# Optimization experiments

Measured on AMD Instinct MI355X. Metric: run time of the kernel, lower is better.

Reference implementation:

```python
import jax, jax.numpy as jnp
import numpy as np

D = 1024   # input_dim
H = 4096   # hidden_dim
E = 8      # num_experts
K = 2      # top_k
LN_EPS = 1e-5


def setup_inputs() -> dict:
    key = jax.random.key(0)
    ks = jax.random.split(key, 6)
    x = jax.random.normal(ks[0], (2, 4096, D), dtype=jnp.float32)
    gate_w = jax.random.normal(ks[1], (D, E), dtype=jnp.float32) * 0.02
    ln_scale = jnp.ones((E, D), dtype=jnp.float32)
    ln_bias = jnp.zeros((E, D), dtype=jnp.float32)
    w1 = jax.random.normal(ks[2], (E, D, H), dtype=jnp.float32) * 0.02
    b1 = jnp.zeros((E, H), dtype=jnp.float32)
    w2 = jax.random.normal(ks[3], (E, H, D), dtype=jnp.float32) * 0.02
    b2 = jnp.zeros((E, D), dtype=jnp.float32)
    return {"x": x, "gate_w": gate_w, "ln_scale": ln_scale, "ln_bias": ln_bias,
            "w1": w1, "b1": b1, "w2": w2, "b2": b2}


def reference(x, gate_w, ln_scale, ln_bias, w1, b1, w2, b2):
    xs = x.reshape(-1, D)                       # [T, D]
    T = xs.shape[0]
    # gating: softmax logits -> top-k -> renormalize selected weights via softmax
    probs = jax.nn.softmax(xs @ gate_w, axis=-1)            # [T, E]
    wts, sel = jax.lax.top_k(probs, K)                      # [T, K]
    wts = jax.nn.softmax(wts, axis=-1).astype(x.dtype)      # [T, K]
    # dense combine weights per (token, expert): 0 if not selected
    comb = jnp.zeros((T, E), dtype=x.dtype).at[jnp.arange(T)[:, None], sel].add(wts)
    # LayerNorm stats are expert-independent; compute once
    mu = xs.mean(-1, keepdims=True)
    var = jnp.mean((xs - mu) ** 2, axis=-1, keepdims=True)
    xn = (xs - mu) * jax.lax.rsqrt(var + LN_EPS)            # [T, D]
    out = jnp.zeros_like(xs)
    for e in range(E):  # small fixed loop over experts
        h = xn * ln_scale[e] + ln_bias[e]                   # [T, D]
        h1 = jax.nn.gelu(h @ w1[e] + b1[e], approximate=False)  # [T, H]
        y = h1 @ w2[e] + b2[e]                              # [T, D]
        out = out + comb[:, e, None] * y
    return out.reshape(x.shape)
```

## Files before the change

### kernel.cpp

```cpp
#include <hip/hip_runtime.h>
#include <hip/hip_bf16.h>
#include <hip/hip_fp16.h>
#include <math.h>

#define T_TOK 8192
#define DIM   1024
#define HID   4096
#define NE    8
#define NT256 72
#define CAP_ROWS (NT256 * 256)

typedef _Float16 f16x8 __attribute__((ext_vector_type(8)));
typedef float    floatx4 __attribute__((ext_vector_type(4)));

__device__ __forceinline__ void gload_lds16(const void* g, void* l) {
    __builtin_amdgcn_global_load_lds(
        (const __attribute__((address_space(1))) void*)g,
        (__attribute__((address_space(3))) void*)l,
        16, 0, 0);
}

__device__ __forceinline__ float gelu_f(float v) {
    float u = v * (0.7978845608028654f + 0.03567740813636141f * v * v);
    float e = exp2f(2.8853900817779268f * u);
    float th = 1.f - 2.f / (e + 1.f);
    return 0.5f * v * (1.f + th);
}

__global__ __launch_bounds__(256) void gating_ln_kernel(
    const float* __restrict__ x, const float* __restrict__ gw,
    int* __restrict__ sel, float* __restrict__ wts,
    float* __restrict__ mu_arr, float* __restrict__ rstd_arr)
{
    int t = blockIdx.x;
    int tid = threadIdx.x;
    float4 xv = ((const float4*)(x + (size_t)t * DIM))[tid];
    float s  = xv.x + xv.y + xv.z + xv.w;
    float ss = xv.x*xv.x + xv.y*xv.y + xv.z*xv.z + xv.w*xv.w;
    float l[NE];
#pragma unroll
    for (int e = 0; e < NE; e++) l[e] = 0.f;
    int d0 = tid * 4;
    const float* xp = &xv.x;
#pragma unroll
    for (int j = 0; j < 4; j++) {
        float xj = xp[j];
        const float4* g = (const float4*)(gw + (size_t)(d0 + j) * NE);
        float4 g0 = g[0], g1 = g[1];
        l[0] += xj * g0.x; l[1] += xj * g0.y; l[2] += xj * g0.z; l[3] += xj * g0.w;
        l[4] += xj * g1.x; l[5] += xj * g1.y; l[6] += xj * g1.z; l[7] += xj * g1.w;
    }
#pragma unroll
    for (int off = 32; off > 0; off >>= 1) {
        s  += __shfl_down(s, off);
        ss += __shfl_down(ss, off);
#pragma unroll
        for (int e = 0; e < NE; e++) l[e] += __shfl_down(l[e], off);
    }
    __shared__ float red[4][10];
    int lane = tid & 63, wv = tid >> 6;
    if (lane == 0) {
        red[wv][0] = s; red[wv][1] = ss;
        for (int e = 0; e < NE; e++) red[wv][2 + e] = l[e];
    }
    __syncthreads();
    if (tid == 0) {
        float S = 0.f, SS = 0.f, L[NE];
        for (int e = 0; e < NE; e++) L[e] = 0.f;
        for (int w = 0; w < 4; w++) {
            S += red[w][0]; SS += red[w][1];
            for (int e = 0; e < NE; e++) L[e] += red[w][2 + e];
        }
        float mu  = S * (1.f / DIM);
        float var = SS * (1.f / DIM) - mu * mu;
        float rstd = rsqrtf(var + 1e-5f);
        float lmax = L[0];
        for (int e = 1; e < NE; e++) lmax = fmaxf(lmax, L[e]);
        float den = 0.f;
        for (int e = 0; e < NE; e++) den += expf(L[e] - lmax);
        int i0 = 0; float b0 = L[0];
        for (int e = 1; e < NE; e++) if (L[e] > b0) { b0 = L[e]; i0 = e; }
        int i1 = -1; float b1v = -3.4e38f;
        for (int e = 0; e < NE; e++) if (e != i0 && L[e] > b1v) { b1v = L[e]; i1 = e; }
        float p0 = expf(b0 - lmax) / den;
        float p1 = expf(b1v - lmax) / den;
        float t1 = expf(p1 - p0);
        float w0 = 1.f / (1.f + t1);
        float w1 = t1 / (1.f + t1);
        sel[2*t] = i0;  sel[2*t+1] = i1;
        wts[2*t] = w0;  wts[2*t+1] = w1;
        mu_arr[t] = mu; rstd_arr[t] = rstd;
    }
}

__global__ __launch_bounds__(256) void hist_kernel(
    const int* __restrict__ sel, int* __restrict__ blockhist,
    unsigned short* __restrict__ lrank)
{
    int b = blockIdx.x, tid = threadIdx.x;
    int t = b * 256 + tid;
    int e0 = sel[2*t], e1 = sel[2*t+1];
    int lane = tid & 63, w = tid >> 6;
    __shared__ int c0[4][NE], c1[4][NE];
    unsigned long long below = (1ull << lane) - 1ull;
    int r0 = 0, r1 = 0;
#pragma unroll
    for (int e = 0; e < NE; e++) {
        unsigned long long m0 = __ballot(e0 == e);
        unsigned long long m1 = __ballot(e1 == e);
        if (lane == 0) { c0[w][e] = __popcll(m0); c1[w][e] = __popcll(m1); }
        if (e0 == e) r0 = __popcll(m0 & below);
        if (e1 == e) r1 = __popcll(m1 & below);
    }
    __syncthreads();
    int base0 = 0, base1 = 0;
#pragma unroll
    for (int wp = 0; wp < 4; wp++) {
        if (wp < w) { base0 += c0[wp][e0]; base1 += c1[wp][e1]; }
        base1 += c0[wp][e1];
    }
    lrank[2*t]   = (unsigned short)(base0 + r0);
    lrank[2*t+1] = (unsigned short)(base1 + r1);
    if (tid < NE) {
        int sum = 0;
        for (int wp = 0; wp < 4; wp++) sum += c0[wp][tid] + c1[wp][tid];
        blockhist[b * NE + tid] = sum;
    }
}

__global__ __launch_bounds__(256) void scan_kernel(
    const int* __restrict__ blockhist, int* __restrict__ off, int* __restrict__ counts,
    int* __restrict__ babs, int* __restrict__ tile_expert)
{
    __shared__ int soff[NE + 1];
    __shared__ int stot[NE];
    int tid = threadIdx.x;
    if (tid < NE) {
        int tot = 0;
        for (int b = 0; b < 32; b++) tot += blockhist[b * NE + tid];
        stot[tid] = tot; counts[tid] = tot;
    }
    __syncthreads();
    if (tid == 0) {
        int o = 0;
        for (int e = 0; e < NE; e++) { soff[e] = o; off[e] = o; o += ((stot[e] + 255) >> 8) << 8; }
        soff[NE] = o; off[NE] = o;
    }
    __syncthreads();
    if (tid < NE) {
        int run = soff[tid];
        for (int b = 0; b < 32; b++) { babs[b * NE + tid] = run; run += blockhist[b * NE + tid]; }
    }
    int o = soff[NE];
    for (int i = tid; i < NT256; i += 256) {
        int pos = i * 256, e = -1;
        if (pos < o) {
            for (int j = 0; j < NE; j++)
                if (pos >= soff[j] && pos < soff[j + 1]) { e = j; break; }
        }
        tile_expert[i] = e;
    }
}

__global__ __launch_bounds__(256) void scatter_kernel(
    const float* __restrict__ x, const float* __restrict__ ln_s, const float* __restrict__ ln_b,
    const int* __restrict__ sel,
    const float* __restrict__ mu_arr, const float* __restrict__ rstd_arr,
    const int* __restrict__ babs, const unsigned short* __restrict__ lrank,
    _Float16* __restrict__ xg, int* __restrict__ slot_of)
{
    int t = blockIdx.x, tid = threadIdx.x;
    int b = t >> 8;
    int e0 = sel[2*t], e1 = sel[2*t+1];
    int s0 = babs[b * NE + e0] + (int)lrank[2*t];
    int s1 = babs[b * NE + e1] + (int)lrank[2*t+1];
    if (tid == 0) { slot_of[2*t] = s0; slot_of[2*t+1] = s1; }
    float4 xv = ((const float4*)(x + (size_t)t * DIM))[tid];
    float mu = mu_arr[t], rstd = rstd_arr[t];
    float xn0 = (xv.x - mu) * rstd, xn1 = (xv.y - mu) * rstd;
    float xn2 = (xv.z - mu) * rstd, xn3 = (xv.w - mu) * rstd;
#pragma unroll
    for (int k = 0; k < 2; k++) {
        int e = (k == 0) ? e0 : e1;
        int slot = (k == 0) ? s0 : s1;
        float4 sv = ((const float4*)(ln_s + (size_t)e * DIM))[tid];
        float4 bv = ((const float4*)(ln_b + (size_t)e * DIM))[tid];
        _Float16 hb[4];
        hb[0] = (_Float16)(xn0 * sv.x + bv.x);
        hb[1] = (_Float16)(xn1 * sv.y + bv.y);
        hb[2] = (_Float16)(xn2 * sv.z + bv.z);
        hb[3] = (_Float16)(xn3 * sv.w + bv.w);
        *(uint2*)(xg + (size_t)slot * DIM + tid * 4) = *(const uint2*)hb;
    }
}

__global__ __launch_bounds__(256) void transpose_cvt_kernel(
    const float* __restrict__ in, _Float16* __restrict__ out, int R, int C)
{
    __shared__ _Float16 tile[64][65];
    size_t ebase = (size_t)blockIdx.z * R * C;
    const float* inp = in + ebase + (size_t)(blockIdx.y * 64) * C + blockIdx.x * 64;
    _Float16* outp = out + ebase + (size_t)(blockIdx.x * 64) * R + blockIdx.y * 64;
    int t = threadIdx.x & 31, j0 = threadIdx.x >> 5;
    for (int j = j0; j < 64; j += 8) {
        float2 v = *(const float2*)(inp + (size_t)j * C + 2 * t);
        tile[j][2*t]   = (_Float16)v.x;
        tile[j][2*t+1] = (_Float16)v.y;
    }
    __syncthreads();
    for (int j = j0; j < 64; j += 8) {
        _Float16 pr[2] = { tile[2*t][j], tile[2*t+1][j] };
        *(unsigned int*)(outp + (size_t)j * R + 2 * t) = *(unsigned int*)pr;
    }
}


#define BAR() __builtin_amdgcn_s_barrier()
#define WAITLGKM() asm volatile("s_waitcnt lgkmcnt(0)" ::: "memory")
#define SCB() __builtin_amdgcn_sched_barrier(0)
#define VMC0() asm volatile("s_waitcnt vmcnt(0)" ::: "memory")
#define VMCN() do { if (LPB == 2) { asm volatile("s_waitcnt vmcnt(6)" ::: "memory"); } \
                    else          { asm volatile("s_waitcnt vmcnt(5)" ::: "memory"); } } while (0)

#define DSA(B_, MHI) do {                                                        \
    const char* p_ = smb + (B_) * (2 * BUFH) + (MHI) * 16384 + aob;              \
    _Pragma("unroll")                                                            \
    for (int mi_ = 0; mi_ < MH; ++mi_) {                                         \
        af[mi_][0] = *(const f16x8*)(p_ + mi_ * 2048 + kx0);                     \
        af[mi_][1] = *(const f16x8*)(p_ + mi_ * 2048 + kx1);                     \
    }                                                                            \
} while (0)

#define DSB(B_, NHI) do {                                                        \
    const char* p_ = smb + (B_) * (2 * BUFH) + (NHI) * (BN * 64) + bob;          \
    _Pragma("unroll")                                                            \
    for (int tn_ = 0; tn_ < 2; ++tn_) {                                          \
        bf[tn_][0] = *(const f16x8*)(p_ + tn_ * 2048 + kx0);                     \
        bf[tn_][1] = *(const f16x8*)(p_ + tn_ * 2048 + kx1);                     \
    }                                                                            \
} while (0)

#define STA(B_, KOFF, H_) do {                                                   \
    _Float16* d_ = smem + (B_) * BUFH + (H_) * 8192 + tid * 8;                   \
    gload_lds16(gA0 + (size_t)((H_) * (WM / 2)) * K + (KOFF), d_);               \
    gload_lds16(gA1 + (size_t)((H_) * (WM / 2)) * K + (KOFF), d_ + 4096);        \
} while (0)

#define STB(B_, KOFF, H_) do {                                                   \
    _Float16* d_ = smem + (B_) * BUFH + 16384 + (H_) * BHH + tid * 8;            \
    gload_lds16(gB0 + (size_t)((H_) * 32) * K + (KOFF), d_);                     \
    if (LPB == 2) gload_lds16(gB1 + (size_t)((H_) * 32) * K + (KOFF), d_ + 4096);\
} while (0)

#define MM(MHI, NHI) do {                                                        \
    _Pragma("unroll")                                                            \
    for (int mi_ = 0; mi_ < MH; ++mi_) {                                         \
        _Pragma("unroll")                                                        \
        for (int tn_ = 0; tn_ < 2; ++tn_) {                                      \
            floatx4* a_ = &acc[(MHI) * MH + mi_][(NHI) * 2 + tn_];               \
            *a_ = __builtin_amdgcn_mfma_f32_16x16x32_f16(af[mi_][0], bf[tn_][0], *a_, 0, 0, 0); \
            *a_ = __builtin_amdgcn_mfma_f32_16x16x32_f16(af[mi_][1], bf[tn_][1], *a_, 0, 0, 0); \
        }                                                                        \
    }                                                                            \
} while (0)

#define PH_MM(MHI, NHI)                                                          \
    BAR(); WAITLGKM(); SCB();                                                    \
    __builtin_amdgcn_s_setprio(1); MM(MHI, NHI); __builtin_amdgcn_s_setprio(0);

#define ITER(SON) do {                                                           \
    DSA(0, 0); DSB(0, 0); STB(1, 64, 0);                                         \
    PH_MM(0, 0) BAR();                                                           \
    DSB(0, 1); if (SON) STA(0, 128, 0);                                          \
    PH_MM(0, 1) BAR();                                                           \
    DSA(0, 1); if (SON) STB(0, 128, 1);                                          \
    PH_MM(1, 1) BAR();                                                           \
    DSB(0, 0); if (SON) STA(0, 128, 1);                                          \
    PH_MM(1, 0) if (SON) { VMCN(); } else { VMC0(); } BAR();                     \
    DSA(1, 0); DSB(1, 0); if (SON) STB(0, 128, 0);                               \
    PH_MM(0, 0) BAR();                                                           \
    DSB(1, 1); if (SON) STA(1, 192, 0);                                          \
    PH_MM(0, 1) BAR();                                                           \
    DSA(1, 1); if (SON) STB(1, 192, 1);                                          \
    PH_MM(1, 1) BAR();                                                           \
    DSB(1, 0); if (SON) STA(1, 192, 1);                                          \
    PH_MM(1, 0) if (SON) { VMCN(); } BAR();                                      \
} while (0)

template <int BN, int NTOT, int K, bool EPI1>
__global__ __launch_bounds__(512, 2) void gemm8p_kernel(
    const _Float16* __restrict__ Ap,
    const _Float16* __restrict__ Bp,
    const float* __restrict__ bias,
    const int* __restrict__ tile_expert,
    const int* __restrict__ off, const int* __restrict__ counts,
    _Float16* __restrict__ h1out, float* __restrict__ yout)
{
    constexpr int WARPS_N = BN / 64;
    constexpr int WM = 256 / (8 / WARPS_N);
    constexpr int MH = WM / 32;
    constexpr int LPB = BN / 128;
    constexpr int BHH = BN * 32;
    constexpr int BUFH = 16384 + BN * 64;
    constexpr int NT_N = NTOT / BN;
    constexpr int NI = K / 128;

    __shared__ _Float16 smem[2 * BUFH];
    const char* smb = (const char*)smem;

    int bid = blockIdx.x;
    constexpr int CHUNK = (NT256 * NT_N) / 8;
    int xcd = bid & 7, slot = bid >> 3;
    int mt, nt;
    if constexpr (NT_N == 16) {
        int sg = slot / 36, w = slot % 36;
        mt = xcd * 9 + (w % 9);
        nt = sg * 4 + (w / 9);
    } else {
        mt = xcd * (CHUNK / NT_N) + slot / NT_N;
        nt = slot % NT_N;
    }
    int e = tile_expert[mt];
    if (e < 0) return;
    int row0 = mt * 256, n0 = nt * BN;

    int tid = threadIdx.x;
    int lane = tid & 63, wv = tid >> 6;
    int wn = wv % WARPS_N, wm = wv / WARPS_N;
    int lm = lane & 15, kq = lane >> 4;
    int kx0 = (kq * 16) ^ ((lm & 7) << 4);
    int kx1 = kx0 ^ 64;
    int aob = (wm * (WM / 2) + lm) * 128;
    int bob = 32768 + (wn * 32 + lm) * 128;

    int trow = tid >> 3;
    int tcol = ((tid & 7) * 16) ^ ((trow & 7) << 4);
    int j1 = trow + 64;
    int oa0 = (trow / (WM / 2)) * WM + (trow % (WM / 2));
    int oa1 = (j1 / (WM / 2)) * WM + (j1 % (WM / 2));
    int ob0 = (trow >> 5) * 64 + (trow & 31);
    int ob1 = (j1 >> 5) * 64 + (j1 & 31);
    const _Float16* gA0 = Ap + ((size_t)(row0 + oa0)) * K + (tcol >> 1);
    const _Float16* gA1 = Ap + ((size_t)(row0 + oa1)) * K + (tcol >> 1);
    const _Float16* gB0 = Bp + ((size_t)e * NTOT + n0 + ob0) * K + (tcol >> 1);
    const _Float16* gB1 = (LPB == 2) ? Bp + ((size_t)e * NTOT + n0 + ob1) * K + (tcol >> 1)
                                     : gB0;

    floatx4 acc[2 * MH][4] = {};
    f16x8 af[MH][2], bf[2][2];

    STA(0, 0, 0); STA(0, 0, 1); STB(0, 0, 0); STB(0, 0, 1);
    STA(1, 64, 0); STB(1, 64, 1); STA(1, 64, 1);
    VMC0(); BAR();

#pragma unroll 1
    for (int i = 0; i < NI - 1; ++i) {
        ITER(1);
        gA0 += 128; gA1 += 128; gB0 += 128; gB1 += 128;
    }
    ITER(0);

    if constexpr (EPI1) {
        const float* be = bias + (size_t)e * NTOT + n0 + wn * 64;
        float bb[4];
#pragma unroll
        for (int ni = 0; ni < 4; ++ni) bb[ni] = be[ni * 16 + lm];
        _Float16* wbuf = smem + wv * (16 * 72);
        int rowg0 = row0 + wm * WM;
        int colg0 = n0 + wn * 64;
#pragma unroll
        for (int mi = 0; mi < 2 * MH; ++mi) {
#pragma unroll
            for (int ni = 0; ni < 4; ++ni)
#pragma unroll
                for (int r = 0; r < 4; ++r)
                    wbuf[(kq * 4 + r) * 72 + ni * 16 + lm] =
                        (_Float16)gelu_f(acc[mi][ni][r] + bb[ni]);
#pragma unroll
            for (int i2 = 0; i2 < 2; ++i2) {
                int idx = i2 * 64 + lane;
                int rr = idx >> 3, cc = (idx & 7) * 8;
                *(f16x8*)(h1out + (size_t)(rowg0 + mi * 16 + rr) * NTOT + colg0 + cc) =
                    *(const f16x8*)(wbuf + rr * 72 + cc);
            }
        }
    } else {
        int end = off[e] + counts[e];
#pragma unroll
        for (int mi = 0; mi < 2 * MH; ++mi) {
            int rbase = row0 + wm * WM + mi * 16 + kq * 4;
#pragma unroll
            for (int r = 0; r < 4; ++r) {
                int s = rbase + r;
                if (s >= end) continue;
#pragma unroll
                for (int ni = 0; ni < 4; ++ni) {
                    int d = n0 + wn * 64 + ni * 16 + lm;
                    yout[(size_t)s * NTOT + d] = acc[mi][ni][r];
                }
            }
        }
    }
}

#undef ITER
#undef PH_MM
#undef MM
#undef STB
#undef STA
#undef DSB
#undef DSA
#undef VMCN
#undef VMC0
#undef SCB
#undef WAITLGKM
#undef BAR

__global__ __launch_bounds__(256) void combine_kernel(
    const float* __restrict__ y, const int* __restrict__ slot_of,
    const float* __restrict__ wts, const int* __restrict__ sel,
    const float* __restrict__ b2, float* __restrict__ out)
{
    int t = blockIdx.x, i = threadIdx.x;
    int s0 = slot_of[2*t], s1 = slot_of[2*t+1];
    int e0 = sel[2*t], e1 = sel[2*t+1];
    float w0 = wts[2*t], w1 = wts[2*t+1];
    float4 y0 = ((const float4*)(y + (size_t)s0 * DIM))[i];
    float4 y1 = ((const float4*)(y + (size_t)s1 * DIM))[i];
    float4 c0 = ((const float4*)(b2 + (size_t)e0 * DIM))[i];
    float4 c1 = ((const float4*)(b2 + (size_t)e1 * DIM))[i];
    float4 o;
    o.x = w0 * (y0.x + c0.x) + w1 * (y1.x + c1.x);
    o.y = w0 * (y0.y + c0.y) + w1 * (y1.y + c1.y);
    o.z = w0 * (y0.z + c0.z) + w1 * (y1.z + c1.z);
    o.w = w0 * (y0.w + c0.w) + w1 * (y1.w + c1.w);
    ((float4*)(out + (size_t)t * DIM))[i] = o;
}

extern "C" void kernel_launch(void* const* d_in, const int* in_sizes, int n_in,
                              void* d_out, int out_size, void* d_ws, size_t ws_size,
                              hipStream_t stream)
{
    const float* x    = (const float*)d_in[0];
    const float* gw   = (const float*)d_in[1];
    const float* ln_s = (const float*)d_in[2];
    const float* ln_b = (const float*)d_in[3];
    const float* w1   = (const float*)d_in[4];
    const float* b1   = (const float*)d_in[5];
    const float* w2   = (const float*)d_in[6];
    const float* b2   = (const float*)d_in[7];
    float* out = (float*)d_out;

    char* p = (char*)d_ws;
    auto carve = [&](size_t bytes) -> char* {
        char* r = p;
        p += (bytes + 255) & ~(size_t)255;
        return r;
    };
    int*   counts    = (int*)carve(NE * 4);
    int*   off       = (int*)carve((NE + 1) * 4);
    int*   tile_exp  = (int*)carve(NT256 * 4);
    int*   blockhist = (int*)carve(32 * NE * 4);
    int*   babs      = (int*)carve(32 * NE * 4);
    int*   sel       = (int*)carve((size_t)T_TOK * 2 * 4);
    float* wts       = (float*)carve((size_t)T_TOK * 2 * 4);
    float* mu_arr    = (float*)carve((size_t)T_TOK * 4);
    float* rstd_arr  = (float*)carve((size_t)T_TOK * 4);
    int*   slot_of   = (int*)carve((size_t)T_TOK * 2 * 4);
    unsigned short* lrank = (unsigned short*)carve((size_t)T_TOK * 2 * 2);
    _Float16* xg  = (_Float16*)carve((size_t)CAP_ROWS * DIM * 2);
    _Float16* w1t = (_Float16*)carve((size_t)NE * DIM * HID * 2);
    _Float16* w2t = (_Float16*)carve((size_t)NE * DIM * HID * 2);
    _Float16* H1  = (_Float16*)carve((size_t)CAP_ROWS * HID * 2);
    float* y = (float*)xg;

    gating_ln_kernel<<<T_TOK, 256, 0, stream>>>(x, gw, sel, wts, mu_arr, rstd_arr);
    hist_kernel<<<32, 256, 0, stream>>>(sel, blockhist, lrank);
    scan_kernel<<<1, 256, 0, stream>>>(blockhist, off, counts, babs, tile_exp);
    scatter_kernel<<<T_TOK, 256, 0, stream>>>(x, ln_s, ln_b, sel, mu_arr, rstd_arr,
                                              babs, lrank, xg, slot_of);
    transpose_cvt_kernel<<<dim3(HID/64, DIM/64, NE), 256, 0, stream>>>(w1, w1t, DIM, HID);
    transpose_cvt_kernel<<<dim3(DIM/64, HID/64, NE), 256, 0, stream>>>(w2, w2t, HID, DIM);

    gemm8p_kernel<256, HID, DIM, true><<<NT256 * (HID / 256), 512, 0, stream>>>(
        xg, w1t, b1, tile_exp, off, counts, H1, nullptr);
    gemm8p_kernel<128, DIM, HID, false><<<NT256 * (DIM / 128), 512, 0, stream>>>(
        H1, w2t, nullptr, tile_exp, off, counts, nullptr, y);

    combine_kernel<<<T_TOK, 256, 0, stream>>>(y, slot_of, wts, sel, b2, out);
}
```

Baseline: 787.5 us.

## Restructure GEMM pipeline into four phases with both B halves in registers

Each k-iteration of the grouped expert GEMM now runs four phases instead of eight. Both N-halves of the B fragments are loaded into registers at once, and each phase issues MFMAs over a full A half. The global-to-LDS prefetch schedule is reordered to match, with adjusted vmcnt waits and a changed prologue load order. The aim is to halve the barrier and waitcnt overhead per iteration and get longer MFMA runs. In exchange it uses more VGPRs for the B fragments and overlaps loads less finely.

```diff
diff --git a/kernel.cpp b/kernel.cpp
--- a/kernel.cpp
+++ b/kernel.cpp
@@ -220,7 +220,7 @@
 #define SCB() __builtin_amdgcn_sched_barrier(0)
 #define VMC0() asm volatile("s_waitcnt vmcnt(0)" ::: "memory")
 #define VMCN() do { if (LPB == 2) { asm volatile("s_waitcnt vmcnt(6)" ::: "memory"); } \
-                    else          { asm volatile("s_waitcnt vmcnt(5)" ::: "memory"); } } while (0)
+                    else          { asm volatile("s_waitcnt vmcnt(4)" ::: "memory"); } } while (0)
 
 #define DSA(B_, MHI) do {                                                        \
     const char* p_ = smb + (B_) * (2 * BUFH) + (MHI) * 16384 + aob;              \
@@ -231,12 +231,15 @@
     }                                                                            \
 } while (0)
 
-#define DSB(B_, NHI) do {                                                        \
-    const char* p_ = smb + (B_) * (2 * BUFH) + (NHI) * (BN * 64) + bob;          \
+#define DSB2(B_) do {                                                            \
     _Pragma("unroll")                                                            \
-    for (int tn_ = 0; tn_ < 2; ++tn_) {                                          \
-        bf[tn_][0] = *(const f16x8*)(p_ + tn_ * 2048 + kx0);                     \
-        bf[tn_][1] = *(const f16x8*)(p_ + tn_ * 2048 + kx1);                     \
+    for (int nh_ = 0; nh_ < 2; ++nh_) {                                          \
+        const char* p_ = smb + (B_) * (2 * BUFH) + nh_ * (BN * 64) + bob;        \
+        _Pragma("unroll")                                                        \
+        for (int tn_ = 0; tn_ < 2; ++tn_) {                                      \
+            bf[nh_][tn_][0] = *(const f16x8*)(p_ + tn_ * 2048 + kx0);            \
+            bf[nh_][tn_][1] = *(const f16x8*)(p_ + tn_ * 2048 + kx1);            \
+        }                                                                        \
     }                                                                            \
 } while (0)
 
@@ -258,33 +261,25 @@
         _Pragma("unroll")                                                        \
         for (int tn_ = 0; tn_ < 2; ++tn_) {                                      \
             floatx4* a_ = &acc[(MHI) * MH + mi_][(NHI) * 2 + tn_];               \
-            *a_ = __builtin_amdgcn_mfma_f32_16x16x32_f16(af[mi_][0], bf[tn_][0], *a_, 0, 0, 0); \
-            *a_ = __builtin_amdgcn_mfma_f32_16x16x32_f16(af[mi_][1], bf[tn_][1], *a_, 0, 0, 0); \
+            *a_ = __builtin_amdgcn_mfma_f32_16x16x32_f16(af[mi_][0], bf[NHI][tn_][0], *a_, 0, 0, 0); \
+            *a_ = __builtin_amdgcn_mfma_f32_16x16x32_f16(af[mi_][1], bf[NHI][tn_][1], *a_, 0, 0, 0); \
         }                                                                        \
     }                                                                            \
 } while (0)
 
-#define PH_MM(MHI, NHI)                                                          \
+#define PH2MM(MHI)                                                               \
     BAR(); WAITLGKM(); SCB();                                                    \
-    __builtin_amdgcn_s_setprio(1); MM(MHI, NHI); __builtin_amdgcn_s_setprio(0);
+    __builtin_amdgcn_s_setprio(1); MM(MHI, 0); MM(MHI, 1); __builtin_amdgcn_s_setprio(0);
 
 #define ITER(SON) do {                                                           \
-    DSA(0, 0); DSB(0, 0); STB(1, 64, 0);                                         \
-    PH_MM(0, 0) BAR();                                                           \
-    DSB(0, 1); if (SON) STA(0, 128, 0);                                          \
-    PH_MM(0, 1) BAR();                                                           \
-    DSA(0, 1); if (SON) STB(0, 128, 1);                                          \
-    PH_MM(1, 1) BAR();                                                           \
-    DSB(0, 0); if (SON) STA(0, 128, 1);                                          \
-    PH_MM(1, 0) if (SON) { VMCN(); } else { VMC0(); } BAR();                     \
-    DSA(1, 0); DSB(1, 0); if (SON) STB(0, 128, 0);                               \
-    PH_MM(0, 0) BAR();                                                           \
-    DSB(1, 1); if (SON) STA(1, 192, 0);                                          \
-    PH_MM(0, 1) BAR();                                                           \
-    DSA(1, 1); if (SON) STB(1, 192, 1);                                          \
-    PH_MM(1, 1) BAR();                                                           \
-    DSB(1, 0); if (SON) STA(1, 192, 1);                                          \
-    PH_MM(1, 0) if (SON) { VMCN(); } BAR();                                      \
+    DSA(0, 0); DSB2(0); STA(1, 64, 1);                                           \
+    PH2MM(0) BAR();                                                              \
+    DSA(0, 1); if (SON) { STA(0, 128, 0); STB(0, 128, 0); STB(0, 128, 1); }      \
+    PH2MM(1) if (SON) { VMCN(); } else { VMC0(); } BAR();                        \
+    DSA(1, 0); DSB2(1); if (SON) STA(0, 128, 1);                                 \
+    PH2MM(0) BAR();                                                              \
+    DSA(1, 1); if (SON) { STA(1, 192, 0); STB(1, 192, 0); STB(1, 192, 1); }      \
+    PH2MM(1) if (SON) { VMCN(); } BAR();                                         \
 } while (0)
 
 template <int BN, int NTOT, int K, bool EPI1>
@@ -347,10 +342,10 @@
                                      : gB0;
 
     floatx4 acc[2 * MH][4] = {};
-    f16x8 af[MH][2], bf[2][2];
+    f16x8 af[MH][2], bf[2][2][2];
 
     STA(0, 0, 0); STA(0, 0, 1); STB(0, 0, 0); STB(0, 0, 1);
-    STA(1, 64, 0); STB(1, 64, 1); STA(1, 64, 1);
+    STA(1, 64, 0); STB(1, 64, 0); STB(1, 64, 1);
     VMC0(); BAR();
 
 #pragma unroll 1
@@ -404,11 +399,11 @@
 }
 
 #undef ITER
-#undef PH_MM
+#undef PH2MM
 #undef MM
 #undef STB
 #undef STA
-#undef DSB
+#undef DSB2
 #undef DSA
 #undef VMCN
 #undef VMC0
```

Result: no change. 790.8 us (+0.4%).
